# Optimization experiments

Measured on AMD Instinct MI355X. Metric: run time of the kernel, lower is better.

## Reference

```python
import jax, jax.numpy as jnp
import numpy as np

B, L, H, V = 16, 512, 256, 32000
HALF = H // 2
EPS_LN = 1e-5
EPS_NORM = 1e-12


def setup_inputs() -> dict:
    key = jax.random.key(0)
    ks = jax.random.split(key, 9)
    s = 0.02
    return {
        "seq": jax.random.randint(ks[0], (B, L), 0, V),
        "embed": jax.random.normal(ks[1], (V, H), jnp.float32) * s,
        "W1": jax.random.normal(ks[2], (2 * H, H), jnp.float32) * s,
        "b1": jnp.zeros((2 * H,), jnp.float32),
        "W2": jax.random.normal(ks[3], (H, 2 * H), jnp.float32) * s,
        "b2": jnp.zeros((H,), jnp.float32),
        "gamma": jnp.ones((H,), jnp.float32),
        "beta": jnp.zeros((H,), jnp.float32),
        "W_sem": jax.random.normal(ks[4], (HALF, H), jnp.float32) * s,
        "W_epi": jax.random.normal(ks[5], (HALF, H), jnp.float32) * s,
        "W_rp": jax.random.normal(ks[6], (H, H), jnp.float32) * s,
        "b_rp": jnp.zeros((H,), jnp.float32),
        "W_out": jax.random.normal(ks[7], (V, H), jnp.float32) * s,
        "b_out": jnp.zeros((V,), jnp.float32),
    }


def _l2norm(x):
    # F.normalize(dim=-1): x / max(||x||, eps)
    n = jnp.sqrt(jnp.sum(x * x, axis=-1, keepdims=True))
    return x / jnp.maximum(n, EPS_NORM)


def reference(seq, embed, W1, b1, W2, b2, gamma, beta, W_sem, W_epi, W_rp, b_rp, W_out, b_out):
    h = embed[seq]                                   # [B, L, H]
    ff = jnp.maximum(h @ W1.T + b1, 0.0) @ W2.T + b2  # MLP with 2H hidden
    x = h + ff
    mu = jnp.mean(x, axis=-1, keepdims=True)
    var = jnp.var(x, axis=-1, keepdims=True)
    h = (x - mu) / jnp.sqrt(var + EPS_LN) * gamma + beta  # LayerNorm

    ks_all = jnp.einsum('blh,kh->blk', h, W_sem)     # [B, L, HALF]
    ke_all = jnp.einsum('blh,kh->blk', h, W_epi)

    def step(carry, kv):
        M_s, M_e = carry
        k_s, k_e = kv                                 # [B, HALF] each
        kns = _l2norm(k_s)
        kne = _l2norm(k_e)
        vps = jnp.einsum('bij,bj->bi', M_s, kns)      # read from fast weights
        vpe = jnp.einsum('bij,bj->bi', M_e, kne)
        M_s = M_s + jnp.einsum('bi,bj->bij', k_s - vps, kns)  # delta-rule write
        M_e = M_e + jnp.einsum('bi,bj->bij', k_e - vpe, kne)
        return (M_s, M_e), None

    M0 = jnp.zeros((B, HALF, HALF), h.dtype)
    # scan over timesteps 0..L-2 (time-major)
    (M_s, M_e), _ = jax.lax.scan(
        step, (M0, M0),
        (jnp.swapaxes(ks_all[:, :-1], 0, 1), jnp.swapaxes(ke_all[:, :-1], 0, 1)))

    cs = jnp.einsum('bij,bj->bi', M_s, ks_all[:, -1])  # read with last-token query
    ce = jnp.einsum('bij,bj->bi', M_e, ke_all[:, -1])
    c = jnp.concatenate([cs, ce], axis=-1)             # [B, H]
    r = c @ W_rp.T + b_rp
    return r @ W_out.T + b_out                          # [B, V]
```

## Files before the change

### kernel.cpp

```cpp
#include <hip/hip_runtime.h>

#define B_ 16
#define L_ 512
#define H_ 256
#define V_ 32000
#define HALF_ 128

typedef __attribute__((ext_vector_type(8))) short short8;
typedef __attribute__((ext_vector_type(4))) float floatx4;

__device__ __forceinline__ unsigned short f2bf(float x) {
  unsigned int u = __float_as_uint(x);
  unsigned int r = (u + 0x7FFFu + ((u >> 16) & 1u)) >> 16;
  return (unsigned short)r;
}

template <int CTRL>
__device__ __forceinline__ float dpp_xor_add(float x) {
  int y = __builtin_amdgcn_mov_dpp(__float_as_int(x), CTRL, 0xf, 0xf, true);
  return x + __int_as_float(y);
}

__device__ __forceinline__ float redu16(float p) {
  p = dpp_xor_add<0xB1>(p);
  p = dpp_xor_add<0x4E>(p);
  p = dpp_xor_add<0x141>(p);
  p = dpp_xor_add<0x140>(p);
  return p;
}

__global__ __launch_bounds__(256) void wconv_kernel(const float* __restrict__ W1,
                                                    const float* __restrict__ W2,
                                                    const float* __restrict__ Ws,
                                                    const float* __restrict__ We,
                                                    unsigned short* __restrict__ W1b,
                                                    unsigned short* __restrict__ W2b,
                                                    unsigned short* __restrict__ Wcb) {
  int i = blockIdx.x * 256 + threadIdx.x;
  if (i < 131072) W1b[i] = f2bf(W1[i]);
  else if (i < 262144) W2b[i - 131072] = f2bf(W2[i - 131072]);
  else if (i < 294912) Wcb[i - 262144] = f2bf(Ws[i - 262144]);
  else Wcb[i - 262144] = f2bf(We[i - 294912]);
}

__device__ __forceinline__ uint4 load8cvt(const float* p) {
  float4 a = ((const float4*)p)[0];
  float4 b = ((const float4*)p)[1];
  uint4 r;
  r.x = (unsigned)f2bf(a.x) | ((unsigned)f2bf(a.y) << 16);
  r.y = (unsigned)f2bf(a.z) | ((unsigned)f2bf(a.w) << 16);
  r.z = (unsigned)f2bf(b.x) | ((unsigned)f2bf(b.y) << 16);
  r.w = (unsigned)f2bf(b.z) | ((unsigned)f2bf(b.w) << 16);
  return r;
}

__global__ __launch_bounds__(256) void gemm1_kernel(const int* __restrict__ seq,
                                                    const float* __restrict__ embed,
                                                    const unsigned short* __restrict__ W1b,
                                                    const float* __restrict__ b1,
                                                    unsigned short* __restrict__ a1b) {
  __shared__ unsigned short As[128 * 40];
  __shared__ unsigned short Bs[128 * 40];
  int tid = threadIdx.x;
  int wave = tid >> 6, lane = tid & 63;
  int wm = (wave >> 1) * 64, wn = (wave & 1) * 64;
  int quad = lane >> 4, l15 = lane & 15;
  int bm = blockIdx.y * 128, bn = blockIdx.x * 128;
  int sr = tid >> 2, sq = tid & 3;

  int tok0 = seq[bm + sr];
  int tok1 = seq[bm + 64 + sr];

  floatx4 zero = {0.f, 0.f, 0.f, 0.f};
  floatx4 acc[2][4];
#pragma unroll
  for (int fi = 0; fi < 2; fi++)
#pragma unroll
    for (int fj = 0; fj < 4; fj++) acc[fi][fj] = zero;
  floatx4 acc2[2][4];
#pragma unroll
  for (int fi = 0; fi < 2; fi++)
#pragma unroll
    for (int fj = 0; fj < 4; fj++) acc2[fi][fj] = zero;

  for (int k0 = 0; k0 < 256; k0 += 32) {
    uint4 av0 = load8cvt(embed + (size_t)tok0 * H_ + k0 + sq * 8);
    uint4 av1 = load8cvt(embed + (size_t)tok1 * H_ + k0 + sq * 8);
    uint4 bv0 = *(const uint4*)(W1b + (size_t)(bn + sr) * 256 + k0 + sq * 8);
    uint4 bv1 = *(const uint4*)(W1b + (size_t)(bn + 64 + sr) * 256 + k0 + sq * 8);
    __syncthreads();
    *(uint4*)(As + sr * 40 + sq * 8) = av0;
    *(uint4*)(As + (64 + sr) * 40 + sq * 8) = av1;
    *(uint4*)(Bs + sr * 40 + sq * 8) = bv0;
    *(uint4*)(Bs + (64 + sr) * 40 + sq * 8) = bv1;
    __syncthreads();
    short8 af[4], bf[4];
#pragma unroll
    for (int f = 0; f < 4; f++) {
      af[f] = *(const short8*)(As + (wm + f * 16 + l15) * 40 + quad * 8);
      bf[f] = *(const short8*)(Bs + (wn + f * 16 + l15) * 40 + quad * 8);
    }
#pragma unroll
    for (int fi = 0; fi < 2; fi++)
#pragma unroll
      for (int fj = 0; fj < 4; fj++) {
        acc[fi][fj] = __builtin_amdgcn_mfma_f32_16x16x32_bf16(af[fi], bf[fj], acc[fi][fj], 0, 0, 0);
        acc2[fi][fj] = __builtin_amdgcn_mfma_f32_16x16x32_bf16(af[fi + 2], bf[fj], acc2[fi][fj], 0, 0, 0);
      }
  }

#pragma unroll
  for (int fi = 0; fi < 4; fi++) {
#pragma unroll
    for (int fj = 0; fj < 4; fj++) {
      int col = bn + wn + fj * 16 + l15;
      float bb = b1[col];
      floatx4 a = (fi < 2) ? acc[fi][fj] : acc2[fi - 2][fj];
#pragma unroll
      for (int rg = 0; rg < 4; rg++) {
        int row = bm + wm + fi * 16 + quad * 4 + rg;
        float v = fmaxf(a[rg] + bb, 0.f);
        a1b[(size_t)row * 512 + col] = f2bf(v);
      }
    }
  }
}

__global__ __launch_bounds__(256) void mlp2_kernel(const unsigned short* __restrict__ a1b,
                                                   const unsigned short* __restrict__ W2b,
                                                   const float* __restrict__ b2,
                                                   const int* __restrict__ seq,
                                                   const float* __restrict__ embed,
                                                   const float* __restrict__ gamma,
                                                   const float* __restrict__ beta,
                                                   unsigned short* __restrict__ hnb) {
  __shared__ unsigned short As[32 * 40];
  __shared__ unsigned short Bs[256 * 40];
  __shared__ float stats[2][2][32];
  int tid = threadIdx.x;
  int wave = tid >> 6, lane = tid & 63;
  int wm = (wave >> 1) * 16, wnh = wave & 1, wn = wnh * 128;
  int quad = lane >> 4, l15 = lane & 15;
  int bm = blockIdx.x * 32;

  floatx4 zero = {0.f, 0.f, 0.f, 0.f};
  floatx4 acc[8];
#pragma unroll
  for (int fj = 0; fj < 8; fj++) acc[fj] = zero;

  for (int k0 = 0; k0 < 512; k0 += 32) {
    uint4 av;
    if (tid < 128) {
      int sr = tid >> 2, sq = tid & 3;
      av = *(const uint4*)(a1b + (size_t)(bm + sr) * 512 + k0 + sq * 8);
    }
    uint4 bv[4];
#pragma unroll
    for (int q = 0; q < 4; q++) {
      int unit = q * 256 + tid;
      int row = unit >> 2, sq2 = unit & 3;
      bv[q] = *(const uint4*)(W2b + (size_t)row * 512 + k0 + sq2 * 8);
    }
    __syncthreads();
    if (tid < 128) {
      int sr = tid >> 2, sq = tid & 3;
      *(uint4*)(As + sr * 40 + sq * 8) = av;
    }
#pragma unroll
    for (int q = 0; q < 4; q++) {
      int unit = q * 256 + tid;
      int row = unit >> 2, sq2 = unit & 3;
      *(uint4*)(Bs + row * 40 + sq2 * 8) = bv[q];
    }
    __syncthreads();
    short8 af = *(const short8*)(As + (wm + l15) * 40 + quad * 8);
    short8 bf[8];
#pragma unroll
    for (int fj = 0; fj < 8; fj++)
      bf[fj] = *(const short8*)(Bs + (wn + fj * 16 + l15) * 40 + quad * 8);
#pragma unroll
    for (int fj = 0; fj < 8; fj++)
      acc[fj] = __builtin_amdgcn_mfma_f32_16x16x32_bf16(af, bf[fj], acc[fj], 0, 0, 0);
  }

  int seqv[4];
#pragma unroll
  for (int rg = 0; rg < 4; rg++) seqv[rg] = seq[bm + wm + quad * 4 + rg];
  float v[8][4];
#pragma unroll
  for (int fj = 0; fj < 8; fj++) {
    int col = wn + fj * 16 + l15;
    float bb = b2[col];
#pragma unroll
    for (int rg = 0; rg < 4; rg++)
      v[fj][rg] = acc[fj][rg] + bb + embed[(size_t)seqv[rg] * H_ + col];
  }
  float s_[4], q_[4];
#pragma unroll
  for (int rg = 0; rg < 4; rg++) {
    float s = 0.f, q = 0.f;
#pragma unroll
    for (int fj = 0; fj < 8; fj++) {
      s += v[fj][rg];
      q += v[fj][rg] * v[fj][rg];
    }
    s_[rg] = redu16(s);
    q_[rg] = redu16(q);
  }
  if (l15 == 0) {
#pragma unroll
    for (int rg = 0; rg < 4; rg++) {
      int rlocal = wm + quad * 4 + rg;
      stats[wnh][0][rlocal] = s_[rg];
      stats[wnh][1][rlocal] = q_[rg];
    }
  }
  __syncthreads();
  float mu[4], inv[4];
#pragma unroll
  for (int rg = 0; rg < 4; rg++) {
    int rlocal = wm + quad * 4 + rg;
    float sum = stats[0][0][rlocal] + stats[1][0][rlocal];
    float ssq = stats[0][1][rlocal] + stats[1][1][rlocal];
    mu[rg] = sum * (1.f / H_);
    float var = ssq * (1.f / H_) - mu[rg] * mu[rg];
    inv[rg] = rsqrtf(var + 1e-5f);
  }
#pragma unroll
  for (int fj = 0; fj < 8; fj++) {
    int col = wn + fj * 16 + l15;
    float g = gamma[col], be = beta[col];
#pragma unroll
    for (int rg = 0; rg < 4; rg++) {
      int row = bm + wm + quad * 4 + rg;
      float y = (v[fj][rg] - mu[rg]) * inv[rg] * g + be;
      hnb[(size_t)row * H_ + col] = f2bf(y);
    }
  }
}

__global__ __launch_bounds__(256) void kproj_kernel(const unsigned short* __restrict__ hnb,
                                                    const unsigned short* __restrict__ Wcb,
                                                    float* __restrict__ khat,
                                                    float* __restrict__ kT) {
  __shared__ unsigned short As[32 * 40];
  __shared__ unsigned short Bs[256 * 40];
  int tid = threadIdx.x;
  int wave = tid >> 6, lane = tid & 63;
  int wm = (wave >> 1) * 16, wnh = wave & 1, wn = wnh * 128;
  int quad = lane >> 4, l15 = lane & 15;
  int bm = blockIdx.x * 32;

  floatx4 zero = {0.f, 0.f, 0.f, 0.f};
  floatx4 acc[8];
#pragma unroll
  for (int fj = 0; fj < 8; fj++) acc[fj] = zero;

  for (int k0 = 0; k0 < 256; k0 += 32) {
    uint4 av;
    if (tid < 128) {
      int sr = tid >> 2, sq = tid & 3;
      av = *(const uint4*)(hnb + (size_t)(bm + sr) * H_ + k0 + sq * 8);
    }
    uint4 bv[4];
#pragma unroll
    for (int q = 0; q < 4; q++) {
      int unit = q * 256 + tid;
      int row = unit >> 2, sq2 = unit & 3;
      bv[q] = *(const uint4*)(Wcb + (size_t)row * H_ + k0 + sq2 * 8);
    }
    __syncthreads();
    if (tid < 128) {
      int sr = tid >> 2, sq = tid & 3;
      *(uint4*)(As + sr * 40 + sq * 8) = av;
    }
#pragma unroll
    for (int q = 0; q < 4; q++) {
      int unit = q * 256 + tid;
      int row = unit >> 2, sq2 = unit & 3;
      *(uint4*)(Bs + row * 40 + sq2 * 8) = bv[q];
    }
    __syncthreads();
    short8 af = *(const short8*)(As + (wm + l15) * 40 + quad * 8);
    short8 bf[8];
#pragma unroll
    for (int fj = 0; fj < 8; fj++)
      bf[fj] = *(const short8*)(Bs + (wn + fj * 16 + l15) * 40 + quad * 8);
#pragma unroll
    for (int fj = 0; fj < 8; fj++)
      acc[fj] = __builtin_amdgcn_mfma_f32_16x16x32_bf16(af, bf[fj], acc[fj], 0, 0, 0);
  }

  int b = bm >> 9;
  int idxm = b * 2 + wnh;
  int tloc0 = (bm & 511) + wm + quad * 4;
  float inv[4];
#pragma unroll
  for (int rg = 0; rg < 4; rg++) {
    float ssq = 0.f;
#pragma unroll
    for (int fj = 0; fj < 8; fj++) ssq += acc[fj][rg] * acc[fj][rg];
    ssq = redu16(ssq);
    inv[rg] = 1.f / fmaxf(sqrtf(ssq), 1e-12f);
  }
#pragma unroll
  for (int fj = 0; fj < 8; fj++) {
    int ch = fj * 16 + l15;
#pragma unroll
    for (int rg = 0; rg < 4; rg++)
      khat[((size_t)idxm * L_ + tloc0 + rg) * HALF_ + ch] = acc[fj][rg] * inv[rg];
    float4 raw = {acc[fj][0], acc[fj][1], acc[fj][2], acc[fj][3]};
    *(float4*)(kT + (size_t)idxm * (HALF_ * L_) + (size_t)ch * L_ + tloc0) = raw;
  }
}

#define STEP8(KP, PR)                                                      \
  do {                                                                     \
    float t0_ = m[0] * KP[0] + m[1] * KP[1];                               \
    float t1_ = m[2] * KP[2] + m[3] * KP[3];                               \
    float t2_ = m[4] * KP[4] + m[5] * KP[5];                               \
    float t3_ = m[6] * KP[6] + m[7] * KP[7];                               \
    float p_ = (t0_ + t1_) + (t2_ + t3_);                                  \
    p_ = redu16(p_);                                                       \
    float s_ = PR - p_;                                                    \
    m[0] += s_ * KP[0]; m[1] += s_ * KP[1]; m[2] += s_ * KP[2];            \
    m[3] += s_ * KP[3]; m[4] += s_ * KP[4]; m[5] += s_ * KP[5];            \
    m[6] += s_ * KP[6]; m[7] += s_ * KP[7];                                \
  } while (0)

__global__ __launch_bounds__(256, 1) void scan_kernel(const float* __restrict__ khat,
                                                      const float* __restrict__ kT,
                                                      float* __restrict__ c) {
  int bid = blockIdx.x;
  int idxm = bid & 31;
  int rg = bid >> 5;
  int b = idxm >> 1, mat = idxm & 1;
  const float* kh = khat + (size_t)idxm * L_ * HALF_;
  const float* kTi = kT + (size_t)idxm * HALF_ * L_;

  int tid = threadIdx.x;
  int seg = tid & 15;
  int rl = tid >> 4;
  int r = rg * 16 + rl;
  int c0 = seg * 8;
  const float* krow = kTi + (size_t)r * L_;

  float m[8];
#pragma unroll
  for (int g = 0; g < 8; g++) m[g] = 0.f;

  float pk[8][8];
  float kr[8];
#pragma unroll
  for (int u = 0; u < 8; u++) {
    *(float4*)&pk[u][0] = *(const float4*)(kh + (size_t)u * HALF_ + c0);
    *(float4*)&pk[u][4] = *(const float4*)(kh + (size_t)u * HALF_ + c0 + 4);
  }
  *(float4*)&kr[0] = *(const float4*)(krow);
  *(float4*)&kr[4] = *(const float4*)(krow + 4);

  for (int i = 0; i < 63; i++) {
    int nt = (i + 1) * 8;
    const float* knext = kh + (size_t)nt * HALF_ + c0;
#pragma unroll
    for (int u = 0; u < 8; u++) {
      STEP8(pk[u], kr[u]);
      *(float4*)&pk[u][0] = *(const float4*)(knext + (size_t)u * HALF_);
      *(float4*)&pk[u][4] = *(const float4*)(knext + (size_t)u * HALF_ + 4);
      if (u == 3) *(float4*)&kr[0] = *(const float4*)(krow + nt);
      if (u == 7) *(float4*)&kr[4] = *(const float4*)(krow + nt + 4);
    }
  }
#pragma unroll
  for (int u = 0; u < 7; u++) STEP8(pk[u], kr[u]);

  float q[8];
#pragma unroll
  for (int j = 0; j < 8; j++) q[j] = kTi[(size_t)(c0 + j) * L_ + 511];
  float t0 = m[0] * q[0] + m[1] * q[1];
  float t1 = m[2] * q[2] + m[3] * q[3];
  float t2 = m[4] * q[4] + m[5] * q[5];
  float t3 = m[6] * q[6] + m[7] * q[7];
  float p = redu16((t0 + t1) + (t2 + t3));
  if (seg == 0) c[(size_t)b * H_ + mat * HALF_ + r] = p;
}

__global__ void rp_kernel(const float* __restrict__ c, const float* __restrict__ Wrp,
                          const float* __restrict__ brp, float* __restrict__ r) {
  int b = blockIdx.x;
  int n = threadIdx.x;
  __shared__ float cs[H_];
  cs[n] = c[(size_t)b * H_ + n];
  __syncthreads();
  const float4* w4 = (const float4*)(Wrp + (size_t)n * H_);
  const float4* c4 = (const float4*)cs;
  float acc = 0.f;
#pragma unroll 8
  for (int k = 0; k < H_ / 4; k++) {
    float4 w = w4[k], cc = c4[k];
    acc += w.x * cc.x + w.y * cc.y + w.z * cc.z + w.w * cc.w;
  }
  r[(size_t)b * H_ + n] = acc + brp[n];
}

__global__ __launch_bounds__(256) void out_kernel(const float* __restrict__ r,
                                                  const float* __restrict__ Wout,
                                                  const float* __restrict__ bout,
                                                  float* __restrict__ out) {
  __shared__ float rs[16 * 272];
  __shared__ float obuf[16 * 68];
  int tid = threadIdx.x;
#pragma unroll
  for (int q = 0; q < 16; q++) {
    int idx = q * 256 + tid;
    int bb = idx >> 8, cc = idx & 255;
    rs[bb * 272 + cc + 4 * (cc >> 6)] = r[idx];
  }
  __syncthreads();
  int row = tid >> 2, part = tid & 3;
  int v = blockIdx.x * 64 + row;
  const float4* w4 = (const float4*)(Wout + (size_t)v * H_ + part * 64);
  float acc[16];
#pragma unroll
  for (int bb = 0; bb < 16; bb++) acc[bb] = 0.f;
#pragma unroll 4
  for (int j = 0; j < 16; j++) {
    float4 w = w4[j];
#pragma unroll
    for (int bb = 0; bb < 16; bb++) {
      float4 rv = *(const float4*)&rs[bb * 272 + part * 68 + j * 4];
      acc[bb] += w.x * rv.x + w.y * rv.y + w.z * rv.z + w.w * rv.w;
    }
  }
  float bo = bout[v];
#pragma unroll
  for (int bb = 0; bb < 16; bb++) {
    acc[bb] = dpp_xor_add<0xB1>(acc[bb]);
    acc[bb] = dpp_xor_add<0x4E>(acc[bb]);
  }
#pragma unroll
  for (int q = 0; q < 4; q++) {
    int bb = part * 4 + q;
    obuf[bb * 68 + row] = acc[bb] + bo;
  }
  __syncthreads();
#pragma unroll
  for (int q = 0; q < 4; q++) {
    int idx = q * 256 + tid;
    int bb = idx >> 6, vl = idx & 63;
    out[(size_t)bb * V_ + blockIdx.x * 64 + vl] = obuf[bb * 68 + vl];
  }
}

extern "C" void kernel_launch(void* const* d_in, const int* in_sizes, int n_in,
                              void* d_out, int out_size, void* d_ws, size_t ws_size,
                              hipStream_t stream) {
  const int* seq = (const int*)d_in[0];
  const float* embed = (const float*)d_in[1];
  const float* W1 = (const float*)d_in[2];
  const float* b1 = (const float*)d_in[3];
  const float* W2 = (const float*)d_in[4];
  const float* b2 = (const float*)d_in[5];
  const float* gamma = (const float*)d_in[6];
  const float* beta = (const float*)d_in[7];
  const float* Wsem = (const float*)d_in[8];
  const float* Wepi = (const float*)d_in[9];
  const float* Wrp = (const float*)d_in[10];
  const float* brp = (const float*)d_in[11];
  const float* Wout = (const float*)d_in[12];
  const float* bout = (const float*)d_in[13];
  float* out = (float*)d_out;

  float* ws = (float*)d_ws;
  unsigned short* a1b = (unsigned short*)ws;
  unsigned short* hnb = (unsigned short*)(ws + 2097152);
  float* khat = ws + 3145728;
  float* kT = ws + 5242880;
  unsigned short* W1b = (unsigned short*)(ws + 7340032);
  unsigned short* W2b = (unsigned short*)(ws + 7405568);
  unsigned short* Wcb = (unsigned short*)(ws + 7471104);
  float* c = ws + 7503872;
  float* r = ws + 7507968;

  wconv_kernel<<<1280, 256, 0, stream>>>(W1, W2, Wsem, Wepi, W1b, W2b, Wcb);
  gemm1_kernel<<<dim3(4, 64), 256, 0, stream>>>(seq, embed, W1b, b1, a1b);
  mlp2_kernel<<<256, 256, 0, stream>>>(a1b, W2b, b2, seq, embed, gamma, beta, hnb);
  kproj_kernel<<<256, 256, 0, stream>>>(hnb, Wcb, khat, kT);
  scan_kernel<<<256, 256, 0, stream>>>(khat, kT, c);
  rp_kernel<<<16, 256, 0, stream>>>(c, Wrp, brp, r);
  out_kernel<<<500, 256, 0, stream>>>(r, Wout, bout, out);
}
```

Baseline: 246.9 us.

## Drop weight-conversion kernel, prefetch GEMM tiles, stage scan keys in LDS asynchronously

Removes the separate fp32-to-bf16 weight conversion kernel and converts weights inline inside the three GEMM kernels. Those GEMM loops now register-prefetch the next K tile while the current one is computed. The scan kernel uses 512-thread blocks covering 32 rows. Its normalized keys are double-buffered into LDS with global_load_lds async copies, and khat is written in a permuted column layout to match. This trades one kernel launch and its global traffic for redundant conversion work per block, and adds LDS pressure and barriers in the latency-bound scan.

New measurement: 243.9 us. Within noise of the previous version (-1.2%).

```diff
diff --git a/kernel.cpp b/kernel.cpp
--- a/kernel.cpp
+++ b/kernel.cpp
@@ -29,18 +29,10 @@
   return p;
 }
 
-__global__ __launch_bounds__(256) void wconv_kernel(const float* __restrict__ W1,
-                                                    const float* __restrict__ W2,
-                                                    const float* __restrict__ Ws,
-                                                    const float* __restrict__ We,
-                                                    unsigned short* __restrict__ W1b,
-                                                    unsigned short* __restrict__ W2b,
-                                                    unsigned short* __restrict__ Wcb) {
-  int i = blockIdx.x * 256 + threadIdx.x;
-  if (i < 131072) W1b[i] = f2bf(W1[i]);
-  else if (i < 262144) W2b[i - 131072] = f2bf(W2[i - 131072]);
-  else if (i < 294912) Wcb[i - 262144] = f2bf(Ws[i - 262144]);
-  else Wcb[i - 262144] = f2bf(We[i - 294912]);
+__device__ __forceinline__ void async_cp16(const float* g, float* l) {
+  __builtin_amdgcn_global_load_lds(
+      (const __attribute__((address_space(1))) void*)g,
+      (__attribute__((address_space(3))) void*)l, 16, 0, 0);
 }
 
 __device__ __forceinline__ uint4 load8cvt(const float* p) {
@@ -56,7 +48,7 @@
 
 __global__ __launch_bounds__(256) void gemm1_kernel(const int* __restrict__ seq,
                                                     const float* __restrict__ embed,
-                                                    const unsigned short* __restrict__ W1b,
+                                                    const float* __restrict__ W1,
                                                     const float* __restrict__ b1,
                                                     unsigned short* __restrict__ a1b) {
   __shared__ unsigned short As[128 * 40];
@@ -72,28 +64,30 @@
   int tok1 = seq[bm + 64 + sr];
 
   floatx4 zero = {0.f, 0.f, 0.f, 0.f};
-  floatx4 acc[2][4];
-#pragma unroll
-  for (int fi = 0; fi < 2; fi++)
+  floatx4 acc[4][4];
+#pragma unroll
+  for (int fi = 0; fi < 4; fi++)
 #pragma unroll
     for (int fj = 0; fj < 4; fj++) acc[fi][fj] = zero;
-  floatx4 acc2[2][4];
-#pragma unroll
-  for (int fi = 0; fi < 2; fi++)
-#pragma unroll
-    for (int fj = 0; fj < 4; fj++) acc2[fi][fj] = zero;
+
+  uint4 av0 = load8cvt(embed + (size_t)tok0 * H_ + sq * 8);
+  uint4 av1 = load8cvt(embed + (size_t)tok1 * H_ + sq * 8);
+  uint4 bv0 = load8cvt(W1 + (size_t)(bn + sr) * 256 + sq * 8);
+  uint4 bv1 = load8cvt(W1 + (size_t)(bn + 64 + sr) * 256 + sq * 8);
 
   for (int k0 = 0; k0 < 256; k0 += 32) {
-    uint4 av0 = load8cvt(embed + (size_t)tok0 * H_ + k0 + sq * 8);
-    uint4 av1 = load8cvt(embed + (size_t)tok1 * H_ + k0 + sq * 8);
-    uint4 bv0 = *(const uint4*)(W1b + (size_t)(bn + sr) * 256 + k0 + sq * 8);
-    uint4 bv1 = *(const uint4*)(W1b + (size_t)(bn + 64 + sr) * 256 + k0 + sq * 8);
     __syncthreads();
     *(uint4*)(As + sr * 40 + sq * 8) = av0;
     *(uint4*)(As + (64 + sr) * 40 + sq * 8) = av1;
     *(uint4*)(Bs + sr * 40 + sq * 8) = bv0;
     *(uint4*)(Bs + (64 + sr) * 40 + sq * 8) = bv1;
     __syncthreads();
+    if (k0 + 32 < 256) {
+      av0 = load8cvt(embed + (size_t)tok0 * H_ + k0 + 32 + sq * 8);
+      av1 = load8cvt(embed + (size_t)tok1 * H_ + k0 + 32 + sq * 8);
+      bv0 = load8cvt(W1 + (size_t)(bn + sr) * 256 + k0 + 32 + sq * 8);
+      bv1 = load8cvt(W1 + (size_t)(bn + 64 + sr) * 256 + k0 + 32 + sq * 8);
+    }
     short8 af[4], bf[4];
 #pragma unroll
     for (int f = 0; f < 4; f++) {
@@ -101,12 +95,10 @@
       bf[f] = *(const short8*)(Bs + (wn + f * 16 + l15) * 40 + quad * 8);
     }
 #pragma unroll
-    for (int fi = 0; fi < 2; fi++)
-#pragma unroll
-      for (int fj = 0; fj < 4; fj++) {
+    for (int fi = 0; fi < 4; fi++)
+#pragma unroll
+      for (int fj = 0; fj < 4; fj++)
         acc[fi][fj] = __builtin_amdgcn_mfma_f32_16x16x32_bf16(af[fi], bf[fj], acc[fi][fj], 0, 0, 0);
-        acc2[fi][fj] = __builtin_amdgcn_mfma_f32_16x16x32_bf16(af[fi + 2], bf[fj], acc2[fi][fj], 0, 0, 0);
-      }
   }
 
 #pragma unroll
@@ -115,11 +107,10 @@
     for (int fj = 0; fj < 4; fj++) {
       int col = bn + wn + fj * 16 + l15;
       float bb = b1[col];
-      floatx4 a = (fi < 2) ? acc[fi][fj] : acc2[fi - 2][fj];
 #pragma unroll
       for (int rg = 0; rg < 4; rg++) {
         int row = bm + wm + fi * 16 + quad * 4 + rg;
-        float v = fmaxf(a[rg] + bb, 0.f);
+        float v = fmaxf(acc[fi][fj][rg] + bb, 0.f);
         a1b[(size_t)row * 512 + col] = f2bf(v);
       }
     }
@@ -127,7 +118,7 @@
 }
 
 __global__ __launch_bounds__(256) void mlp2_kernel(const unsigned short* __restrict__ a1b,
-                                                   const unsigned short* __restrict__ W2b,
+                                                   const float* __restrict__ W2,
                                                    const float* __restrict__ b2,
                                                    const int* __restrict__ seq,
                                                    const float* __restrict__ embed,
@@ -142,37 +133,38 @@
   int wm = (wave >> 1) * 16, wnh = wave & 1, wn = wnh * 128;
   int quad = lane >> 4, l15 = lane & 15;
   int bm = blockIdx.x * 32;
+  int sr = tid >> 2, sq = tid & 3;
 
   floatx4 zero = {0.f, 0.f, 0.f, 0.f};
   floatx4 acc[8];
 #pragma unroll
   for (int fj = 0; fj < 8; fj++) acc[fj] = zero;
 
+  uint4 av, bv[4];
+  if (tid < 128) av = *(const uint4*)(a1b + (size_t)(bm + sr) * 512 + sq * 8);
+#pragma unroll
+  for (int q = 0; q < 4; q++) {
+    int unit = q * 256 + tid;
+    bv[q] = load8cvt(W2 + (size_t)(unit >> 2) * 512 + (unit & 3) * 8);
+  }
+
   for (int k0 = 0; k0 < 512; k0 += 32) {
-    uint4 av;
-    if (tid < 128) {
-      int sr = tid >> 2, sq = tid & 3;
-      av = *(const uint4*)(a1b + (size_t)(bm + sr) * 512 + k0 + sq * 8);
-    }
-    uint4 bv[4];
+    __syncthreads();
+    if (tid < 128) *(uint4*)(As + sr * 40 + sq * 8) = av;
 #pragma unroll
     for (int q = 0; q < 4; q++) {
       int unit = q * 256 + tid;
-      int row = unit >> 2, sq2 = unit & 3;
-      bv[q] = *(const uint4*)(W2b + (size_t)row * 512 + k0 + sq2 * 8);
-    }
-    __syncthreads();
-    if (tid < 128) {
-      int sr = tid >> 2, sq = tid & 3;
-      *(uint4*)(As + sr * 40 + sq * 8) = av;
-    }
-#pragma unroll
-    for (int q = 0; q < 4; q++) {
-      int unit = q * 256 + tid;
-      int row = unit >> 2, sq2 = unit & 3;
-      *(uint4*)(Bs + row * 40 + sq2 * 8) = bv[q];
-    }
-    __syncthreads();
+      *(uint4*)(Bs + (unit >> 2) * 40 + (unit & 3) * 8) = bv[q];
+    }
+    __syncthreads();
+    if (k0 + 32 < 512) {
+      if (tid < 128) av = *(const uint4*)(a1b + (size_t)(bm + sr) * 512 + k0 + 32 + sq * 8);
+#pragma unroll
+      for (int q = 0; q < 4; q++) {
+        int unit = q * 256 + tid;
+        bv[q] = load8cvt(W2 + (size_t)(unit >> 2) * 512 + k0 + 32 + (unit & 3) * 8);
+      }
+    }
     short8 af = *(const short8*)(As + (wm + l15) * 40 + quad * 8);
     short8 bf[8];
 #pragma unroll
@@ -240,7 +232,8 @@
 }
 
 __global__ __launch_bounds__(256) void kproj_kernel(const unsigned short* __restrict__ hnb,
-                                                    const unsigned short* __restrict__ Wcb,
+                                                    const float* __restrict__ Ws,
+                                                    const float* __restrict__ We,
                                                     float* __restrict__ khat,
                                                     float* __restrict__ kT) {
   __shared__ unsigned short As[32 * 40];
@@ -250,37 +243,42 @@
   int wm = (wave >> 1) * 16, wnh = wave & 1, wn = wnh * 128;
   int quad = lane >> 4, l15 = lane & 15;
   int bm = blockIdx.x * 32;
+  int sr = tid >> 2, sq = tid & 3;
 
   floatx4 zero = {0.f, 0.f, 0.f, 0.f};
   floatx4 acc[8];
 #pragma unroll
   for (int fj = 0; fj < 8; fj++) acc[fj] = zero;
 
+  uint4 av, bv[4];
+  if (tid < 128) av = *(const uint4*)(hnb + (size_t)(bm + sr) * H_ + sq * 8);
+#pragma unroll
+  for (int q = 0; q < 4; q++) {
+    int unit = q * 256 + tid;
+    int row = unit >> 2;
+    const float* src = (row < 128) ? (Ws + (size_t)row * H_) : (We + (size_t)(row - 128) * H_);
+    bv[q] = load8cvt(src + (unit & 3) * 8);
+  }
+
   for (int k0 = 0; k0 < 256; k0 += 32) {
-    uint4 av;
-    if (tid < 128) {
-      int sr = tid >> 2, sq = tid & 3;
-      av = *(const uint4*)(hnb + (size_t)(bm + sr) * H_ + k0 + sq * 8);
-    }
-    uint4 bv[4];
+    __syncthreads();
+    if (tid < 128) *(uint4*)(As + sr * 40 + sq * 8) = av;
 #pragma unroll
     for (int q = 0; q < 4; q++) {
       int unit = q * 256 + tid;
-      int row = unit >> 2, sq2 = unit & 3;
-      bv[q] = *(const uint4*)(Wcb + (size_t)row * H_ + k0 + sq2 * 8);
-    }
-    __syncthreads();
-    if (tid < 128) {
-      int sr = tid >> 2, sq = tid & 3;
-      *(uint4*)(As + sr * 40 + sq * 8) = av;
-    }
-#pragma unroll
-    for (int q = 0; q < 4; q++) {
-      int unit = q * 256 + tid;
-      int row = unit >> 2, sq2 = unit & 3;
-      *(uint4*)(Bs + row * 40 + sq2 * 8) = bv[q];
-    }
-    __syncthreads();
+      *(uint4*)(Bs + (unit >> 2) * 40 + (unit & 3) * 8) = bv[q];
+    }
+    __syncthreads();
+    if (k0 + 32 < 256) {
+      if (tid < 128) av = *(const uint4*)(hnb + (size_t)(bm + sr) * H_ + k0 + 32 + sq * 8);
+#pragma unroll
+      for (int q = 0; q < 4; q++) {
+        int unit = q * 256 + tid;
+        int row = unit >> 2;
+        const float* src = (row < 128) ? (Ws + (size_t)row * H_) : (We + (size_t)(row - 128) * H_);
+        bv[q] = load8cvt(src + k0 + 32 + (unit & 3) * 8);
+      }
+    }
     short8 af = *(const short8*)(As + (wm + l15) * 40 + quad * 8);
     short8 bf[8];
 #pragma unroll
@@ -306,42 +304,46 @@
 #pragma unroll
   for (int fj = 0; fj < 8; fj++) {
     int ch = fj * 16 + l15;
+    int j = ch >> 2, e = ch & 3;
+    int pj = (j & 1) ? (16 + (j >> 1)) : (j >> 1);
+    int pcol = pj * 4 + e;
 #pragma unroll
     for (int rg = 0; rg < 4; rg++)
-      khat[((size_t)idxm * L_ + tloc0 + rg) * HALF_ + ch] = acc[fj][rg] * inv[rg];
+      khat[((size_t)idxm * L_ + tloc0 + rg) * HALF_ + pcol] = acc[fj][rg] * inv[rg];
     float4 raw = {acc[fj][0], acc[fj][1], acc[fj][2], acc[fj][3]};
     *(float4*)(kT + (size_t)idxm * (HALF_ * L_) + (size_t)ch * L_ + tloc0) = raw;
   }
 }
 
-#define STEP8(KP, PR)                                                      \
-  do {                                                                     \
-    float t0_ = m[0] * KP[0] + m[1] * KP[1];                               \
-    float t1_ = m[2] * KP[2] + m[3] * KP[3];                               \
-    float t2_ = m[4] * KP[4] + m[5] * KP[5];                               \
-    float t3_ = m[6] * KP[6] + m[7] * KP[7];                               \
-    float p_ = (t0_ + t1_) + (t2_ + t3_);                                  \
-    p_ = redu16(p_);                                                       \
-    float s_ = PR - p_;                                                    \
-    m[0] += s_ * KP[0]; m[1] += s_ * KP[1]; m[2] += s_ * KP[2];            \
-    m[3] += s_ * KP[3]; m[4] += s_ * KP[4]; m[5] += s_ * KP[5];            \
-    m[6] += s_ * KP[6]; m[7] += s_ * KP[7];                                \
+#define STEP(KP, KR)                                                     \
+  do {                                                                   \
+    float t0_ = m[0] * KP[0] + m[1] * KP[1];                             \
+    float t1_ = m[2] * KP[2] + m[3] * KP[3];                             \
+    float t2_ = m[4] * KP[4] + m[5] * KP[5];                             \
+    float t3_ = m[6] * KP[6] + m[7] * KP[7];                             \
+    float p_ = (t0_ + t1_) + (t2_ + t3_);                                \
+    p_ = redu16(p_);                                                     \
+    float s_ = (KR) - p_;                                                \
+    m[0] += s_ * KP[0]; m[1] += s_ * KP[1]; m[2] += s_ * KP[2];          \
+    m[3] += s_ * KP[3]; m[4] += s_ * KP[4]; m[5] += s_ * KP[5];          \
+    m[6] += s_ * KP[6]; m[7] += s_ * KP[7];                              \
   } while (0)
 
-__global__ __launch_bounds__(256, 1) void scan_kernel(const float* __restrict__ khat,
-                                                      const float* __restrict__ kT,
-                                                      float* __restrict__ c) {
+__global__ __launch_bounds__(512) void scan_kernel(const float* __restrict__ khat,
+                                                   const float* __restrict__ kT,
+                                                   float* __restrict__ c) {
+  __shared__ float sk[2][64 * 128];
   int bid = blockIdx.x;
   int idxm = bid & 31;
-  int rg = bid >> 5;
+  int rgp = bid >> 5;
   int b = idxm >> 1, mat = idxm & 1;
   const float* kh = khat + (size_t)idxm * L_ * HALF_;
   const float* kTi = kT + (size_t)idxm * HALF_ * L_;
 
   int tid = threadIdx.x;
-  int seg = tid & 15;
-  int rl = tid >> 4;
-  int r = rg * 16 + rl;
+  int wave = tid >> 6, lane = tid & 63;
+  int seg = tid & 15, rl = tid >> 4;
+  int r = rgp * 32 + rl;
   int c0 = seg * 8;
   const float* krow = kTi + (size_t)r * L_;
 
@@ -349,30 +351,80 @@
 #pragma unroll
   for (int g = 0; g < 8; g++) m[g] = 0.f;
 
-  float pk[8][8];
-  float kr[8];
-#pragma unroll
-  for (int u = 0; u < 8; u++) {
-    *(float4*)&pk[u][0] = *(const float4*)(kh + (size_t)u * HALF_ + c0);
-    *(float4*)&pk[u][4] = *(const float4*)(kh + (size_t)u * HALF_ + c0 + 4);
-  }
-  *(float4*)&kr[0] = *(const float4*)(krow);
-  *(float4*)&kr[4] = *(const float4*)(krow + 4);
-
-  for (int i = 0; i < 63; i++) {
-    int nt = (i + 1) * 8;
-    const float* knext = kh + (size_t)nt * HALF_ + c0;
-#pragma unroll
-    for (int u = 0; u < 8; u++) {
-      STEP8(pk[u], kr[u]);
-      *(float4*)&pk[u][0] = *(const float4*)(knext + (size_t)u * HALF_);
-      *(float4*)&pk[u][4] = *(const float4*)(knext + (size_t)u * HALF_ + 4);
-      if (u == 3) *(float4*)&kr[0] = *(const float4*)(krow + nt);
-      if (u == 7) *(float4*)&kr[4] = *(const float4*)(krow + nt + 4);
-    }
-  }
-#pragma unroll
-  for (int u = 0; u < 7; u++) STEP8(pk[u], kr[u]);
+  {
+#pragma unroll
+    for (int j = 0; j < 4; j++) {
+      int slice = j * 8 + wave;
+      async_cp16(kh + slice * 256 + lane * 4, &sk[0][slice * 256] + lane * 4);
+    }
+  }
+  __syncthreads();
+
+  float4 krn = *(const float4*)(krow);
+  const float* lb = &sk[0][0] + seg * 4;
+
+  for (int ch = 0; ch < 7; ch++) {
+    {
+#pragma unroll
+      for (int j = 0; j < 4; j++) {
+        int slice = j * 8 + wave;
+        async_cp16(kh + (size_t)(ch + 1) * 8192 + slice * 256 + lane * 4,
+                   &sk[(ch + 1) & 1][slice * 256] + lane * 4);
+      }
+    }
+    const float* base = lb + (ch & 1) * 8192;
+    float pk[4][8];
+#pragma unroll
+    for (int u = 0; u < 4; u++) {
+      *(float4*)&pk[u][0] = *(const float4*)(base + u * 128);
+      *(float4*)&pk[u][4] = *(const float4*)(base + u * 128 + 64);
+    }
+    for (int g = 0; g < 15; g++) {
+      float4 krc = krn;
+      krn = *(const float4*)(krow + ch * 64 + g * 4 + 4);
+#pragma unroll
+      for (int u = 0; u < 4; u++) {
+        STEP(pk[u], ((u == 0) ? krc.x : (u == 1) ? krc.y : (u == 2) ? krc.z : krc.w));
+        int tn = g * 4 + u + 4;
+        *(float4*)&pk[u][0] = *(const float4*)(base + tn * 128);
+        *(float4*)&pk[u][4] = *(const float4*)(base + tn * 128 + 64);
+      }
+    }
+    {
+      float4 krc = krn;
+      krn = *(const float4*)(krow + ch * 64 + 64);
+      STEP(pk[0], krc.x);
+      STEP(pk[1], krc.y);
+      STEP(pk[2], krc.z);
+      STEP(pk[3], krc.w);
+    }
+    __syncthreads();
+  }
+
+  {
+    const float* base = lb + 8192;
+    float pk[4][8];
+#pragma unroll
+    for (int u = 0; u < 4; u++) {
+      *(float4*)&pk[u][0] = *(const float4*)(base + u * 128);
+      *(float4*)&pk[u][4] = *(const float4*)(base + u * 128 + 64);
+    }
+    for (int g = 0; g < 15; g++) {
+      float4 krc = krn;
+      krn = *(const float4*)(krow + 448 + g * 4 + 4);
+#pragma unroll
+      for (int u = 0; u < 4; u++) {
+        STEP(pk[u], ((u == 0) ? krc.x : (u == 1) ? krc.y : (u == 2) ? krc.z : krc.w));
+        int tn = g * 4 + u + 4;
+        *(float4*)&pk[u][0] = *(const float4*)(base + tn * 128);
+        *(float4*)&pk[u][4] = *(const float4*)(base + tn * 128 + 64);
+      }
+    }
+    float4 krc = krn;
+    STEP(pk[0], krc.x);
+    STEP(pk[1], krc.y);
+    STEP(pk[2], krc.z);
+  }
 
   float q[8];
 #pragma unroll
@@ -476,17 +528,13 @@
   unsigned short* hnb = (unsigned short*)(ws + 2097152);
   float* khat = ws + 3145728;
   float* kT = ws + 5242880;
-  unsigned short* W1b = (unsigned short*)(ws + 7340032);
-  unsigned short* W2b = (unsigned short*)(ws + 7405568);
-  unsigned short* Wcb = (unsigned short*)(ws + 7471104);
-  float* c = ws + 7503872;
-  float* r = ws + 7507968;
-
-  wconv_kernel<<<1280, 256, 0, stream>>>(W1, W2, Wsem, Wepi, W1b, W2b, Wcb);
-  gemm1_kernel<<<dim3(4, 64), 256, 0, stream>>>(seq, embed, W1b, b1, a1b);
-  mlp2_kernel<<<256, 256, 0, stream>>>(a1b, W2b, b2, seq, embed, gamma, beta, hnb);
-  kproj_kernel<<<256, 256, 0, stream>>>(hnb, Wcb, khat, kT);
-  scan_kernel<<<256, 256, 0, stream>>>(khat, kT, c);
+  float* c = ws + 7340032;
+  float* r = ws + 7344128;
+
+  gemm1_kernel<<<dim3(4, 64), 256, 0, stream>>>(seq, embed, W1, b1, a1b);
+  mlp2_kernel<<<256, 256, 0, stream>>>(a1b, W2, b2, seq, embed, gamma, beta, hnb);
+  kproj_kernel<<<256, 256, 0, stream>>>(hnb, Wsem, Wepi, khat, kT);
+  scan_kernel<<<128, 512, 0, stream>>>(khat, kT, c);
   rp_kernel<<<16, 256, 0, stream>>>(c, Wrp, brp, r);
   out_kernel<<<500, 256, 0, stream>>>(r, Wout, bout, out);
 }
```
